# Kernel tuning notes

Hardware: AMD Instinct MI355X
Metric: run time of the kernel (lower is better)

Reference implementation:

```python
import jax, jax.numpy as jnp
import numpy as np

HIDDEN = 4096
NUM_HEADS = 32
NUM_KV_HEADS = 8
HEAD_DIM = HIDDEN // NUM_HEADS  # 128
ROPE_THETA = 10000.0
T = 2048


def setup_inputs() -> dict:
    key = jax.random.key(0)
    k1, k2, k3 = jax.random.split(key, 3)
    positions = jnp.arange(T, dtype=jnp.int32)
    hidden_states = jax.random.normal(k1, (T, HIDDEN), dtype=jnp.float32)
    # 0.02 init scale keeps logits in a sane range
    Wqkv = jax.random.normal(k2, (HIDDEN, (NUM_HEADS + 2 * NUM_KV_HEADS) * HEAD_DIM), dtype=jnp.float32) * 0.02
    Wo = jax.random.normal(k3, (HIDDEN, HIDDEN), dtype=jnp.float32) * 0.02
    return {"positions": positions, "hidden_states": hidden_states, "Wqkv": Wqkv, "Wo": Wo}


def _rope_neox(x, positions):
    # x: [T, H, D]; neox style rotates halves of the head dim
    d2 = HEAD_DIM // 2
    inv_freq = ROPE_THETA ** (-jnp.arange(0, d2, dtype=jnp.float32) / d2)
    ang = positions.astype(jnp.float32)[:, None] * inv_freq  # [T, d2]
    cos = jnp.cos(ang)[:, None, :]  # [T,1,d2]
    sin = jnp.sin(ang)[:, None, :]
    x1, x2 = x[..., :d2], x[..., d2:]
    return jnp.concatenate([x1 * cos - x2 * sin, x2 * cos + x1 * sin], axis=-1)


def reference(positions, hidden_states, Wqkv, Wo):
    Tn = hidden_states.shape[0]
    q_sz = NUM_HEADS * HEAD_DIM
    kv_sz = NUM_KV_HEADS * HEAD_DIM
    qkv = hidden_states @ Wqkv  # [T, q_sz + 2*kv_sz]
    q = qkv[:, :q_sz].reshape(Tn, NUM_HEADS, HEAD_DIM)
    k = qkv[:, q_sz:q_sz + kv_sz].reshape(Tn, NUM_KV_HEADS, HEAD_DIM)
    v = qkv[:, q_sz + kv_sz:].reshape(Tn, NUM_KV_HEADS, HEAD_DIM)
    q = _rope_neox(q, positions)
    k = _rope_neox(k, positions)
    # GQA: repeat kv heads to match q heads
    rep = NUM_HEADS // NUM_KV_HEADS
    k = jnp.repeat(k, rep, axis=1)  # [T, H, D]
    v = jnp.repeat(v, rep, axis=1)
    scale = HEAD_DIM ** -0.5
    scores = jnp.einsum('thd,shd->hts', q, k) * scale  # [H, T, T]
    causal = positions[:, None] >= positions[None, :]  # [T, T]
    scores = jnp.where(causal[None, :, :], scores, jnp.float32(-1e30))
    probs = jax.nn.softmax(scores, axis=-1)
    attn = jnp.einsum('hts,shd->thd', probs, v).reshape(Tn, HIDDEN)
    return attn @ Wo
```

## Files before the change

### kernel.cpp

```cpp
#include <hip/hip_runtime.h>
#include <hip/hip_bf16.h>
#include <math.h>

#define T_SEQ 2048
#define HID   4096
#define NH    32
#define NKV   8
#define HD    128
#define QKVD  6144
#define KOFF  4096
#define VOFF  5120

typedef unsigned short u16;
typedef unsigned int   u32;
typedef __attribute__((ext_vector_type(4))) float f32x4;
typedef __attribute__((ext_vector_type(8))) short s16x8;
typedef __attribute__((ext_vector_type(4))) unsigned short u16x4;

__device__ inline u16 f2bf(float f) {
  u32 u = __float_as_uint(f);
  u32 r = u + 0x7FFFu + ((u >> 16) & 1u);
  return (u16)(r >> 16);
}
__device__ inline float bf2f(u16 h) { return __uint_as_float(((u32)h) << 16); }

__device__ inline void gl_lds16(const void* g, void* l) {
  __builtin_amdgcn_global_load_lds((const __attribute__((address_space(1))) void*)g,
                                   (__attribute__((address_space(3))) void*)l, 16, 0, 0);
}

__global__ void cast_f32_bf16(const float* __restrict__ in, u16* __restrict__ out, int n) {
  int i = (blockIdx.x * blockDim.x + threadIdx.x) * 4;
  if (i < n) {
    float4 v = *(const float4*)(in + i);
    u16x4 o = { f2bf(v.x), f2bf(v.y), f2bf(v.z), f2bf(v.w) };
    *(u16x4*)(out + i) = o;
  }
}

__global__ void transpose_cast(const float* __restrict__ in, u16* __restrict__ out, int K, int N) {
  __shared__ float tile[32][33];
  int n0 = blockIdx.x * 32, k0 = blockIdx.y * 32;
  int tx = threadIdx.x, ty = threadIdx.y;
  for (int i = ty; i < 32; i += 8)
    tile[i][tx] = in[(size_t)(k0 + i) * N + n0 + tx];
  __syncthreads();
  for (int i = ty; i < 32; i += 8)
    out[(size_t)(n0 + i) * K + k0 + tx] = f2bf(tile[tx][i]);
}

__global__ void vtrans(const u16* __restrict__ qkv, u16* __restrict__ Vt) {
  __shared__ u16 tile[32][33];
  int kv = blockIdx.z;
  int t0 = blockIdx.x * 32, d0 = blockIdx.y * 32;
  int tx = threadIdx.x, ty = threadIdx.y;
  for (int i = ty; i < 32; i += 8)
    tile[i][tx] = qkv[(size_t)(t0 + i) * QKVD + VOFF + kv * HD + d0 + tx];
  __syncthreads();
  for (int i = ty; i < 32; i += 8)
    Vt[(size_t)(kv * HD + d0 + i) * T_SEQ + t0 + tx] = tile[tx][i];
}

__global__ void rope_kernel(u16* __restrict__ qkv, const int* __restrict__ positions) {
  int t = blockIdx.x;
  int h = blockIdx.y * 4 + (threadIdx.x >> 6);
  int i = threadIdx.x & 63;
  float pos = (float)positions[t];
  float freq = exp2f(-(float)i * (13.287712379549449f / 64.0f));
  float ang = pos * freq;
  float s, c;
  sincosf(ang, &s, &c);
  size_t off;
  if (h < NH) off = (size_t)t * QKVD + h * HD;
  else        off = (size_t)t * QKVD + KOFF + (h - NH) * HD;
  float x1 = bf2f(qkv[off + i]);
  float x2 = bf2f(qkv[off + 64 + i]);
  qkv[off + i]      = f2bf(x1 * c - x2 * s);
  qkv[off + 64 + i] = f2bf(x2 * c + x1 * s);
}

template <bool BF16OUT>
__global__ __launch_bounds__(256) void gemm_bt(const u16* __restrict__ A, const u16* __restrict__ B,
                                               void* __restrict__ Cv, int M, int N, int K) {
  __shared__ __align__(16) u16 As[128 * 32];
  __shared__ __align__(16) u16 Bs[128 * 32];
  const int tid = threadIdx.x;
  const int w = tid >> 6, l = tid & 63;
  const int wr = w >> 1, wc = w & 1;
  const int lr = l & 15, lg = l >> 4;
  const int m0 = blockIdx.y * 128, n0 = blockIdx.x * 128;

  f32x4 acc[4][4] = {};

  const int r0 = w * 16 + (l >> 2);
  const int c0 = (l & 3) * 8;
  const u16* pA0 = A + (size_t)(m0 + r0) * K + c0;
  const u16* pA1 = A + (size_t)(m0 + 64 + r0) * K + c0;
  const u16* pB0 = B + (size_t)(n0 + r0) * K + c0;
  const u16* pB1 = B + (size_t)(n0 + 64 + r0) * K + c0;
  u16* dA0 = As + (w * 64) * 8;
  u16* dA1 = As + (256 + w * 64) * 8;
  u16* dB0 = Bs + (w * 64) * 8;
  u16* dB1 = Bs + (256 + w * 64) * 8;

  for (int k0 = 0; k0 < K; k0 += 32) {
    gl_lds16(pA0 + k0, dA0);
    gl_lds16(pA1 + k0, dA1);
    gl_lds16(pB0 + k0, dB0);
    gl_lds16(pB1 + k0, dB1);
    __syncthreads();
    s16x8 af[4], bfr[4];
#pragma unroll
    for (int i = 0; i < 4; i++) {
      af[i]  = *(const s16x8*)(As + (wr * 64 + i * 16 + lr) * 32 + lg * 8);
      bfr[i] = *(const s16x8*)(Bs + (wc * 64 + i * 16 + lr) * 32 + lg * 8);
    }
#pragma unroll
    for (int i = 0; i < 4; i++)
#pragma unroll
      for (int j = 0; j < 4; j++)
        acc[i][j] = __builtin_amdgcn_mfma_f32_16x16x32_bf16(af[i], bfr[j], acc[i][j], 0, 0, 0);
    __syncthreads();
  }
#pragma unroll
  for (int i = 0; i < 4; i++)
#pragma unroll
    for (int j = 0; j < 4; j++)
#pragma unroll
      for (int r = 0; r < 4; r++) {
        int row = m0 + wr * 64 + i * 16 + lg * 4 + r;
        int col = n0 + wc * 64 + j * 16 + lr;
        float v = acc[i][j][r];
        if (BF16OUT) ((u16*)Cv)[(size_t)row * N + col] = f2bf(v);
        else         ((float*)Cv)[(size_t)row * N + col] = v;
      }
}

__device__ inline void stage_tiles(const u16* __restrict__ qkv, const u16* __restrict__ Vt,
                                   u16* Kb, u16* Vb, int kv0, int hkv, int w, int l) {
  const int krow_l = l >> 4;
  const int kcb = (l & 15) << 4;
  const int vrow_l = l >> 3;
  const int vcb = (l & 7) << 4;
#pragma unroll
  for (int c = 0; c < 4; c++) {
    int row = c * 16 + w * 4 + krow_l;
    const char* src = (const char*)(qkv + (size_t)(kv0 + row) * QKVD + KOFF + hkv * HD) +
                      (kcb ^ ((row & 7) << 4));
    gl_lds16(src, (char*)Kb + (c * 16 + w * 4) * 256);
  }
#pragma unroll
  for (int c = 0; c < 4; c++) {
    int row = c * 32 + w * 8 + vrow_l;
    const char* src = (const char*)(Vt + (size_t)(hkv * HD + row) * T_SEQ + kv0) +
                      (vcb ^ ((row & 7) << 4));
    gl_lds16(src, (char*)Vb + (c * 32 + w * 8) * 128);
  }
}

__global__ __launch_bounds__(256) void attn_fwd(const u16* __restrict__ qkv, const u16* __restrict__ Vt,
                                                u16* __restrict__ attnout) {
  __shared__ __align__(16) u16 Ks[2][64 * 128];
  __shared__ __align__(16) u16 Vs[2][128 * 64];
  __shared__ __align__(16) u16 plds[4][16 * 72];
  const int tid = threadIdx.x;
  const int w = tid >> 6, l = tid & 63;
  const int lr = l & 15, g = l >> 4;
  const int h = blockIdx.y;
  const int hkv = h >> 2;
  const int swzl = (lr & 7) << 4;
  const float scale = 0.08838834764831845f;
  u16* pw = &plds[w][0];

  for (int seg = 0; seg < 2; seg++) {
    const int qt = (seg == 0) ? blockIdx.x : (31 - blockIdx.x);
    const int q0 = qt * 64 + w * 16;
    const int q_abs = q0 + lr;

    s16x8 qf[4];
    const u16* qbase = qkv + (size_t)(q0 + lr) * QKVD + h * HD + g * 8;
#pragma unroll
    for (int kk = 0; kk < 4; kk++) qf[kk] = *(const s16x8*)(qbase + kk * 32);

    f32x4 acc_o[8] = {};
    float m_run = -__builtin_inff();
    float l_run = 0.0f;
    const int nt = qt + 1;

    stage_tiles(qkv, Vt, Ks[0], Vs[0], 0, hkv, w, l);
    asm volatile("s_waitcnt vmcnt(0)" ::: "memory");
    __syncthreads();
    int cur = 0;
    for (int kt = 0; kt < nt; kt++) {
      const int kv0 = kt * 64;
      if (kt + 1 < nt)
        stage_tiles(qkv, Vt, Ks[cur ^ 1], Vs[cur ^ 1], kv0 + 64, hkv, w, l);
      const bool masked = (kt == qt);

      f32x4 sa[4];
      const char* kb = (const char*)Ks[cur];
#pragma unroll
      for (int ct = 0; ct < 4; ct++) {
        f32x4 a = {0.f, 0.f, 0.f, 0.f};
#pragma unroll
        for (int kk = 0; kk < 4; kk++) {
          s16x8 kf = *(const s16x8*)(kb + (ct * 16 + lr) * 256 + (((kk << 6) + (g << 4)) ^ swzl));
          a = __builtin_amdgcn_mfma_f32_16x16x32_bf16(kf, qf[kk], a, 0, 0, 0);
        }
        sa[ct] = a;
      }

      float p[16];
      float pmax = -__builtin_inff();
#pragma unroll
      for (int ct = 0; ct < 4; ct++)
#pragma unroll
        for (int r = 0; r < 4; r++) {
          float s = sa[ct][r] * scale;
          if (masked) {
            int kv_abs = kv0 + ct * 16 + g * 4 + r;
            if (kv_abs > q_abs) s = -__builtin_inff();
          }
          p[ct * 4 + r] = s;
          pmax = fmaxf(pmax, s);
        }
      pmax = fmaxf(pmax, __shfl_xor(pmax, 16, 64));
      pmax = fmaxf(pmax, __shfl_xor(pmax, 32, 64));
      float m_new = fmaxf(m_run, pmax);
      float fac = __expf(m_run - m_new);
      float psum = 0.f;
#pragma unroll
      for (int x = 0; x < 16; x++) {
        float e = __expf(p[x] - m_new);
        p[x] = e;
        psum += e;
      }
      psum += __shfl_xor(psum, 16, 64);
      psum += __shfl_xor(psum, 32, 64);
      l_run = l_run * fac + psum;
      m_run = m_new;
      float fr[4];
#pragma unroll
      for (int r = 0; r < 4; r++) fr[r] = __shfl(fac, g * 4 + r, 64);
#pragma unroll
      for (int dt = 0; dt < 8; dt++)
#pragma unroll
        for (int r = 0; r < 4; r++) acc_o[dt][r] *= fr[r];

#pragma unroll
      for (int ct = 0; ct < 4; ct++) {
        u16x4 pk = { f2bf(p[ct * 4 + 0]), f2bf(p[ct * 4 + 1]), f2bf(p[ct * 4 + 2]), f2bf(p[ct * 4 + 3]) };
        *(u16x4*)(pw + lr * 72 + ct * 16 + g * 4) = pk;
      }
      asm volatile("s_waitcnt lgkmcnt(0)" ::: "memory");
      __builtin_amdgcn_sched_barrier(0);
      s16x8 pa0 = *(const s16x8*)(pw + lr * 72 + g * 8);
      s16x8 pa1 = *(const s16x8*)(pw + lr * 72 + 32 + g * 8);

      const char* vbb = (const char*)Vs[cur];
#pragma unroll
      for (int dt = 0; dt < 8; dt++) {
        s16x8 v0 = *(const s16x8*)(vbb + (dt * 16 + lr) * 128 + ((g << 4) ^ swzl));
        s16x8 v1 = *(const s16x8*)(vbb + (dt * 16 + lr) * 128 + ((64 + (g << 4)) ^ swzl));
        acc_o[dt] = __builtin_amdgcn_mfma_f32_16x16x32_bf16(pa0, v0, acc_o[dt], 0, 0, 0);
        acc_o[dt] = __builtin_amdgcn_mfma_f32_16x16x32_bf16(pa1, v1, acc_o[dt], 0, 0, 0);
      }
      asm volatile("s_waitcnt vmcnt(0)" ::: "memory");
      __syncthreads();
      cur ^= 1;
    }

    float ln[4];
#pragma unroll
    for (int r = 0; r < 4; r++) ln[r] = __shfl(l_run, g * 4 + r, 64);
#pragma unroll
    for (int dt = 0; dt < 8; dt++)
#pragma unroll
      for (int r = 0; r < 4; r++) {
        int row = q0 + g * 4 + r;
        int col = h * HD + dt * 16 + lr;
        attnout[(size_t)row * HID + col] = f2bf(acc_o[dt][r] / ln[r]);
      }
  }
}

extern "C" void kernel_launch(void* const* d_in, const int* in_sizes, int n_in,
                              void* d_out, int out_size, void* d_ws, size_t ws_size,
                              hipStream_t stream) {
  const int*   positions = (const int*)d_in[0];
  const float* X         = (const float*)d_in[1];
  const float* Wqkv      = (const float*)d_in[2];
  const float* Wo        = (const float*)d_in[3];
  float* out = (float*)d_out;

  char* ws = (char*)d_ws;
  size_t off = 0;
  u16* Xbf    = (u16*)(ws + off); off += (size_t)T_SEQ * HID * 2;
  u16* Wqkvt  = (u16*)(ws + off); off += (size_t)QKVD * HID * 2;
  u16* Wot    = (u16*)(ws + off); off += (size_t)HID * HID * 2;
  u16* qkv    = (u16*)(ws + off); off += (size_t)T_SEQ * QKVD * 2;
  u16* Vt     = (u16*)(ws + off); off += (size_t)NKV * HD * T_SEQ * 2;
  u16* attnb  = (u16*)(ws + off); off += (size_t)T_SEQ * HID * 2;

  cast_f32_bf16<<<dim3((T_SEQ * HID) / (256 * 4)), dim3(256), 0, stream>>>(X, Xbf, T_SEQ * HID);
  transpose_cast<<<dim3(QKVD / 32, HID / 32), dim3(32, 8), 0, stream>>>(Wqkv, Wqkvt, HID, QKVD);
  transpose_cast<<<dim3(HID / 32, HID / 32), dim3(32, 8), 0, stream>>>(Wo, Wot, HID, HID);
  gemm_bt<true><<<dim3(QKVD / 128, T_SEQ / 128), dim3(256), 0, stream>>>(Xbf, Wqkvt, qkv, T_SEQ, QKVD, HID);
  rope_kernel<<<dim3(T_SEQ, 10), dim3(256), 0, stream>>>(qkv, positions);
  vtrans<<<dim3(T_SEQ / 32, HD / 32, NKV), dim3(32, 8), 0, stream>>>(qkv, Vt);
  attn_fwd<<<dim3(16, 32), dim3(256), 0, stream>>>(qkv, Vt, attnb);
  gemm_bt<false><<<dim3(HID / 128, T_SEQ / 128), dim3(256), 0, stream>>>(attnb, Wot, out, T_SEQ, HID, HID);
}
```

Before: 580.5 us.

## Replace GEMM with 256x256 tiled, double-buffered, swizzled-LDS pipelined kernel

Replaces the simple 128x128 GEMM, which loaded a K-step of 32 and synchronised twice per step, with a 512-thread 256x256 tile kernel. It uses K-steps of 64, double-buffered LDS with XOR swizzle, and staged prefetch of the next A/B halves interleaved between four MFMA quadrants, using s_setprio and explicit vmcnt waits. The aim is to hide global-load latency, raise data reuse per block and cut LDS bank conflicts in both projection GEMMs. In exchange it uses far more LDS and registers and fewer blocks (192 and 128 tiles), which may underfill the 256 CUs.

```diff
diff --git a/kernel.cpp b/kernel.cpp
--- a/kernel.cpp
+++ b/kernel.cpp
@@ -79,62 +79,124 @@
   qkv[off + 64 + i] = f2bf(x2 * c + x1 * s);
 }
 
+__device__ inline void stage_half(const u16* __restrict__ G, int K, u16* lds, int w, int l) {
+  const int rl = l >> 3;
+  const int cs = ((l & 7) ^ rl) << 3;
+#pragma unroll
+  for (int i = 0; i < 2; i++) {
+    const u16* src = G + (size_t)(8 * w + 64 * i + rl) * K + cs;
+    gl_lds16(src, lds + (8 * w + 64 * i) * 64);
+  }
+}
+
+#define LDA(i, kk) a[i][kk] = *(const s16x8*)(Ah + (((i) * 16 + lr) * 64) + ((((kk) * 4 + lg) ^ xsw) << 3))
+#define LDB(j, kk) b[j][kk] = *(const s16x8*)(Bh + (((j) * 16 + lr) * 64) + ((((kk) * 4 + lg) ^ xsw) << 3))
+#define MFMA_Q(i0, j0)                                                        \
+  _Pragma("unroll") for (int i = 0; i < 4; i++)                               \
+  _Pragma("unroll") for (int j = 0; j < 2; j++)                               \
+  _Pragma("unroll") for (int kk = 0; kk < 2; kk++)                            \
+    acc[i0 + i][j0 + j] = __builtin_amdgcn_mfma_f32_16x16x32_bf16(            \
+        a[i0 + i][kk], b[j0 + j][kk], acc[i0 + i][j0 + j], 0, 0, 0);
+
 template <bool BF16OUT>
-__global__ __launch_bounds__(256) void gemm_bt(const u16* __restrict__ A, const u16* __restrict__ B,
-                                               void* __restrict__ Cv, int M, int N, int K) {
-  __shared__ __align__(16) u16 As[128 * 32];
-  __shared__ __align__(16) u16 Bs[128 * 32];
+__global__ __launch_bounds__(512, 2) void gemm256(const u16* __restrict__ A,
+                                                  const u16* __restrict__ B,
+                                                  void* __restrict__ Cv,
+                                                  int M, int N, int K) {
+  __shared__ __align__(16) u16 As[2][2][128 * 64];
+  __shared__ __align__(16) u16 Bs[2][2][128 * 64];
   const int tid = threadIdx.x;
   const int w = tid >> 6, l = tid & 63;
-  const int wr = w >> 1, wc = w & 1;
   const int lr = l & 15, lg = l >> 4;
-  const int m0 = blockIdx.y * 128, n0 = blockIdx.x * 128;
-
-  f32x4 acc[4][4] = {};
-
-  const int r0 = w * 16 + (l >> 2);
-  const int c0 = (l & 3) * 8;
-  const u16* pA0 = A + (size_t)(m0 + r0) * K + c0;
-  const u16* pA1 = A + (size_t)(m0 + 64 + r0) * K + c0;
-  const u16* pB0 = B + (size_t)(n0 + r0) * K + c0;
-  const u16* pB1 = B + (size_t)(n0 + 64 + r0) * K + c0;
-  u16* dA0 = As + (w * 64) * 8;
-  u16* dA1 = As + (256 + w * 64) * 8;
-  u16* dB0 = Bs + (w * 64) * 8;
-  u16* dB1 = Bs + (256 + w * 64) * 8;
-
-  for (int k0 = 0; k0 < K; k0 += 32) {
-    gl_lds16(pA0 + k0, dA0);
-    gl_lds16(pA1 + k0, dA1);
-    gl_lds16(pB0 + k0, dB0);
-    gl_lds16(pB1 + k0, dB1);
-    __syncthreads();
-    s16x8 af[4], bfr[4];
-#pragma unroll
-    for (int i = 0; i < 4; i++) {
-      af[i]  = *(const s16x8*)(As + (wr * 64 + i * 16 + lr) * 32 + lg * 8);
-      bfr[i] = *(const s16x8*)(Bs + (wc * 64 + i * 16 + lr) * 32 + lg * 8);
+  const int wm = w >> 2, wn = w & 3;
+  const int xsw = lr & 7;
+  const int bm = blockIdx.y * 256, bn = blockIdx.x * 256;
+  const int NT = K >> 6;
+
+  const u16* Ab0 = A + (size_t)bm * K;
+  const u16* Ab1 = A + (size_t)(bm + 128) * K;
+  const u16* Bb0 = B + (size_t)bn * K;
+  const u16* Bb1 = B + (size_t)(bn + 128) * K;
+
+  f32x4 acc[8][4] = {};
+
+  stage_half(Ab0, K, As[0][0], w, l);
+  stage_half(Ab1, K, As[0][1], w, l);
+  stage_half(Bb0, K, Bs[0][0], w, l);
+  stage_half(Bb1, K, Bs[0][1], w, l);
+  if (NT > 1) {
+    stage_half(Ab0 + 64, K, As[1][0], w, l);
+    stage_half(Ab1 + 64, K, As[1][1], w, l);
+    asm volatile("s_waitcnt vmcnt(4)" ::: "memory");
+  } else {
+    asm volatile("s_waitcnt vmcnt(0)" ::: "memory");
+  }
+  __builtin_amdgcn_s_barrier();
+
+  for (int t = 0; t < NT; t++) {
+    const int cur = t & 1;
+    const u16* Ah = &As[cur][wm][0];
+    const u16* Bh = &Bs[cur][wn >> 1][(wn & 1) * 64 * 64];
+    s16x8 a[8][2], b[4][2];
+
+#pragma unroll
+    for (int i = 0; i < 4; i++) { LDA(i, 0); LDA(i, 1); }
+    LDB(0, 0); LDB(0, 1); LDB(1, 0); LDB(1, 1);
+    if (t + 1 < NT) stage_half(Bb0 + (size_t)(t + 1) * 64, K, Bs[cur ^ 1][0], w, l);
+    __builtin_amdgcn_s_barrier();
+    asm volatile("s_waitcnt lgkmcnt(0)" ::: "memory");
+    __builtin_amdgcn_s_setprio(1);
+    MFMA_Q(0, 0)
+    __builtin_amdgcn_s_setprio(0);
+    __builtin_amdgcn_s_barrier();
+
+#pragma unroll
+    for (int i = 4; i < 8; i++) { LDA(i, 0); LDA(i, 1); }
+    LDB(2, 0); LDB(2, 1); LDB(3, 0); LDB(3, 1);
+    if (t + 1 < NT) stage_half(Bb1 + (size_t)(t + 1) * 64, K, Bs[cur ^ 1][1], w, l);
+    __builtin_amdgcn_s_barrier();
+    asm volatile("s_waitcnt lgkmcnt(0)" ::: "memory");
+    __builtin_amdgcn_s_setprio(1);
+    MFMA_Q(0, 2)
+    __builtin_amdgcn_s_setprio(0);
+    __builtin_amdgcn_s_barrier();
+
+    if (t + 2 < NT) stage_half(Ab0 + (size_t)(t + 2) * 64, K, As[cur][0], w, l);
+    __builtin_amdgcn_s_barrier();
+    __builtin_amdgcn_s_setprio(1);
+    MFMA_Q(4, 2)
+    __builtin_amdgcn_s_setprio(0);
+    __builtin_amdgcn_s_barrier();
+
+    if (t + 2 < NT) {
+      stage_half(Ab1 + (size_t)(t + 2) * 64, K, As[cur][1], w, l);
+      asm volatile("s_waitcnt vmcnt(4)" ::: "memory");
+    } else {
+      asm volatile("s_waitcnt vmcnt(0)" ::: "memory");
     }
-#pragma unroll
-    for (int i = 0; i < 4; i++)
-#pragma unroll
-      for (int j = 0; j < 4; j++)
-        acc[i][j] = __builtin_amdgcn_mfma_f32_16x16x32_bf16(af[i], bfr[j], acc[i][j], 0, 0, 0);
-    __syncthreads();
-  }
-#pragma unroll
-  for (int i = 0; i < 4; i++)
+    __builtin_amdgcn_s_barrier();
+    __builtin_amdgcn_s_setprio(1);
+    MFMA_Q(4, 0)
+    __builtin_amdgcn_s_setprio(0);
+    __builtin_amdgcn_s_barrier();
+  }
+
+#pragma unroll
+  for (int i = 0; i < 8; i++)
 #pragma unroll
     for (int j = 0; j < 4; j++)
 #pragma unroll
       for (int r = 0; r < 4; r++) {
-        int row = m0 + wr * 64 + i * 16 + lg * 4 + r;
-        int col = n0 + wc * 64 + j * 16 + lr;
+        int row = bm + wm * 128 + i * 16 + lg * 4 + r;
+        int col = bn + wn * 64 + j * 16 + lr;
         float v = acc[i][j][r];
         if (BF16OUT) ((u16*)Cv)[(size_t)row * N + col] = f2bf(v);
         else         ((float*)Cv)[(size_t)row * N + col] = v;
       }
 }
+#undef LDA
+#undef LDB
+#undef MFMA_Q
 
 __device__ inline void stage_tiles(const u16* __restrict__ qkv, const u16* __restrict__ Vt,
                                    u16* Kb, u16* Vb, int kv0, int hkv, int w, int l) {
@@ -201,13 +263,13 @@
       const char* kb = (const char*)Ks[cur];
 #pragma unroll
       for (int ct = 0; ct < 4; ct++) {
-        f32x4 a = {0.f, 0.f, 0.f, 0.f};
+        f32x4 aa = {0.f, 0.f, 0.f, 0.f};
 #pragma unroll
         for (int kk = 0; kk < 4; kk++) {
           s16x8 kf = *(const s16x8*)(kb + (ct * 16 + lr) * 256 + (((kk << 6) + (g << 4)) ^ swzl));
-          a = __builtin_amdgcn_mfma_f32_16x16x32_bf16(kf, qf[kk], a, 0, 0, 0);
+          aa = __builtin_amdgcn_mfma_f32_16x16x32_bf16(kf, qf[kk], aa, 0, 0, 0);
         }
-        sa[ct] = a;
+        sa[ct] = aa;
       }
 
       float p[16];
@@ -305,9 +367,9 @@
   cast_f32_bf16<<<dim3((T_SEQ * HID) / (256 * 4)), dim3(256), 0, stream>>>(X, Xbf, T_SEQ * HID);
   transpose_cast<<<dim3(QKVD / 32, HID / 32), dim3(32, 8), 0, stream>>>(Wqkv, Wqkvt, HID, QKVD);
   transpose_cast<<<dim3(HID / 32, HID / 32), dim3(32, 8), 0, stream>>>(Wo, Wot, HID, HID);
-  gemm_bt<true><<<dim3(QKVD / 128, T_SEQ / 128), dim3(256), 0, stream>>>(Xbf, Wqkvt, qkv, T_SEQ, QKVD, HID);
+  gemm256<true><<<dim3(QKVD / 256, T_SEQ / 256), dim3(512), 0, stream>>>(Xbf, Wqkvt, qkv, T_SEQ, QKVD, HID);
   rope_kernel<<<dim3(T_SEQ, 10), dim3(256), 0, stream>>>(qkv, positions);
   vtrans<<<dim3(T_SEQ / 32, HD / 32, NKV), dim3(32, 8), 0, stream>>>(qkv, Vt);
   attn_fwd<<<dim3(16, 32), dim3(256), 0, stream>>>(qkv, Vt, attnb);
-  gemm_bt<false><<<dim3(HID / 128, T_SEQ / 128), dim3(256), 0, stream>>>(attnb, Wot, out, T_SEQ, HID, HID);
-}
+  gemm256<false><<<dim3(HID / 256, T_SEQ / 256), dim3(512), 0, stream>>>(attnb, Wot, out, T_SEQ, HID, HID);
+}
```

After: 585.7 us. No clear change (+0.9%).
